# Performance work log

Measured on AMD Instinct MI355X. Metric: run time of the kernel, lower is better.

## Reference

```python
import jax, jax.numpy as jnp
import numpy as np

NEG_INF = -9e15  # matches the source's -9000000000000000.0 mask fill
ALPHA = 0.2      # leaky_relu negative slope


def setup_inputs() -> dict:
    key = jax.random.key(0)
    k1, k2, k3, k4 = jax.random.split(key, 4)
    B, N, C_IN, C_OUT, H = 2, 2048, 128, 128, 16
    c = C_OUT // H  # 8 per-head features; equals H//2 so source's a-slice is consistent
    node_feats = jax.random.normal(k1, (B, N, C_IN), dtype=jnp.float32)
    # random 0/1 adjacency with self-loops
    adj = jax.random.randint(k2, (B, N, N), 0, 2).astype(jnp.float32)
    adj = jnp.maximum(adj, jnp.eye(N, dtype=jnp.float32)[None])
    # glorot-uniform-ish params
    W = jax.random.normal(k3, (C_IN, H * c), dtype=jnp.float32) * np.sqrt(2.0 / (C_IN + H * c))
    b = jnp.zeros((H * c,), dtype=jnp.float32)
    a = jax.random.normal(k4, (H, 2 * c), dtype=jnp.float32) * np.sqrt(2.0 / (H + 2 * c))
    return {"node_feats": node_feats, "adj_matrix": adj, "W": W, "b": b, "a": a}


def reference(node_feats, adj_matrix, W, b, a):
    B, N = node_feats.shape[:2]
    H = a.shape[0]
    c = a.shape[1] // 2
    # projection + split into heads: [B, N, H, c]
    h = (node_feats @ W + b).reshape(B, N, H, c)
    # additive attention halves (source slices a along last axis)
    logit_parent = jnp.einsum('bnhc,hc->bnh', h, a[:, :c])
    logit_child = jnp.einsum('bnhc,hc->bnh', h, a[:, c:])
    # dense broadcast-add logits: [B, N(i), N(j), H]
    attn_logits = logit_parent[:, :, None, :] + logit_child[:, None, :, :]
    attn_logits = jax.nn.leaky_relu(attn_logits, negative_slope=ALPHA)
    attn_logits = jnp.where(adj_matrix[..., None] == 1.0, attn_logits, NEG_INF)
    attn_probs = jax.nn.softmax(attn_logits, axis=2)  # over source nodes j
    out = jnp.einsum('bijh,bjhc->bihc', attn_probs, h)
    out = out.reshape(B, N, H * c)  # concat_heads=True
    return out, adj_matrix
```

## Files before the change

### kernel.cpp

```cpp
#include <hip/hip_runtime.h>
#include <hip/hip_bf16.h>


#define B_   2
#define N_   2048
#define CIN_ 128
#define H_   16

typedef _Float16 h2  __attribute__((ext_vector_type(2)));
typedef _Float16 v8h __attribute__((ext_vector_type(8)));
typedef float    v4f __attribute__((ext_vector_type(4)));

#define SC6 0.015625f

__device__ inline h2 pk_f16(float a, float b) {
  return __builtin_bit_cast(h2, __builtin_amdgcn_cvt_pkrtz(a, b));
}
__device__ inline unsigned as_u32(h2 v) { return __builtin_bit_cast(unsigned, v); }
__device__ inline h2 as_h2(unsigned u) { return __builtin_bit_cast(h2, u); }

__device__ inline unsigned mask4(float4 f) {
  unsigned r = (unsigned)f.x | ((unsigned)f.y << 8) |
               ((unsigned)f.z << 16) | ((unsigned)f.w << 24);
  return (r << 8) - r;
}

__global__ __launch_bounds__(128) void proj_kernel(
    const float* __restrict__ nf, const float* __restrict__ W,
    const float* __restrict__ bias, const float* __restrict__ a,
    unsigned* __restrict__ hQ, unsigned* __restrict__ qI,
    float* __restrict__ lpT, unsigned* __restrict__ ones) {
  const int row0 = blockIdx.x * 4;
  const int t    = threadIdx.x;
  if (blockIdx.x == 0) {
    ones[t] = 0x3C003C00u; ones[t + 128] = 0x3C003C00u;
    ones[t + 256] = 0x3C003C00u; ones[t + 384] = 0x3C003C00u;
  }
  __shared__ float sNf[4][CIN_];
  ((float4*)&sNf[0][0])[t] = ((const float4*)(nf + (long)row0 * CIN_))[t];
  __syncthreads();
  float acc[4];
  const float bv = bias[t];
#pragma unroll
  for (int r = 0; r < 4; ++r) acc[r] = bv;
#pragma unroll 8
  for (int k = 0; k < CIN_; ++k) {
    const float w = W[k * 128 + t];
#pragma unroll
    for (int r = 0; r < 4; ++r) acc[r] = fmaf(sNf[r][k], w, acc[r]);
  }
  const int h = t >> 3, kc = t & 7;
  const int b = row0 >> 11, n0 = row0 & (N_ - 1);
  const int bh = b * H_ + h;
  const int cdw = n0 >> 1;
  uint2 hv;
  hv.x = as_u32(pk_f16(acc[0], acc[1]));
  hv.y = as_u32(pk_f16(acc[2], acc[3]));
  *(uint2*)(hQ + ((long)(bh * 8 + kc)) * (N_ / 2) + cdw) = hv;

  const float ap = a[h * 16 + kc], ac = a[h * 16 + 8 + kc];
  float lpv[4], lcv[4];
#pragma unroll
  for (int r = 0; r < 4; ++r) {
    float x = acc[r] * ap, y = acc[r] * ac;
#pragma unroll
    for (int s = 1; s < 8; s <<= 1) {
      x += __shfl_xor(x, s);
      y += __shfl_xor(y, s);
    }
    lpv[r] = x; lcv[r] = y;
  }
  if (kc == 0) {
    float4 l0 = {lpv[0], lpv[1], lpv[2], lpv[3]};
    *(float4*)(lpT + (long)bh * N_ + n0) = l0;
    uint2 q1, q2;
    q1.x = as_u32(pk_f16(__expf(lcv[0]) * SC6, __expf(lcv[1]) * SC6));
    q1.y = as_u32(pk_f16(__expf(lcv[2]) * SC6, __expf(lcv[3]) * SC6));
    q2.x = as_u32(pk_f16(__expf(0.2f * lcv[0]) * SC6, __expf(0.2f * lcv[1]) * SC6));
    q2.y = as_u32(pk_f16(__expf(0.2f * lcv[2]) * SC6, __expf(0.2f * lcv[3]) * SC6));
    const int addr = bh * 2048 + (cdw >> 4) * 32 + ((cdw >> 2) & 3) * 8;
    const int off  = cdw & 3;
    *(uint2*)(qI + addr + off)     = q1;
    *(uint2*)(qI + addr + 4 + off) = q2;
  }
}

__global__ __launch_bounds__(512, 6) void attn_kernel(
    const float* __restrict__ adj, const unsigned* __restrict__ hQ,
    const unsigned* __restrict__ qI, const float* __restrict__ lpT,
    const unsigned* __restrict__ ones, float* __restrict__ pA,
    float* __restrict__ pL, float* __restrict__ adj_out) {
  const int jq   = blockIdx.x & 3;
  const int rest = blockIdx.x >> 2;
  const int b    = rest >> 7;
  const int i0   = (rest & 127) * 16;
  const int tid  = threadIdx.x;
  const int w    = tid >> 6;
  const int lane = tid & 63;

  __shared__ uint2    sAm[1024];
  __shared__ unsigned sQ[8192];

  {
    const int head = tid >> 5;
    const int off  = (tid & 31) * 16;
    const uint4* src = (const uint4*)(qI + (b * H_ + head) * 2048 + jq * 512 + off);
    uint4* dst = (uint4*)(sQ + head * 512 + off);
    dst[0] = src[0]; dst[1] = src[1]; dst[2] = src[2]; dst[3] = src[3];
  }
  {
    const long aoff = (long)(b * N_ + i0) * N_ + jq * 512;
    const float* abase = adj + aoff;
    float* obase = adj_out + aoff;
    float4 fa[2], fb[2];
    int rowv[2], ccv[2];
#pragma unroll
    for (int s = 0; s < 2; ++s) {
      const int D = s * 512 + tid;
      const int mm = D & 15, qc = D >> 4;
      ccv[s] = (qc >> 2) * 32 + (qc & 3) * 8;
      rowv[s] = mm;
      fa[s] = *(const float4*)(abase + (long)mm * N_ + ccv[s]);
      fb[s] = *(const float4*)(abase + (long)mm * N_ + ccv[s] + 4);
    }
#pragma unroll
    for (int s = 0; s < 2; ++s) {
      const int D = s * 512 + tid;
      uint2 mv; mv.x = mask4(fa[s]); mv.y = mask4(fb[s]);
      sAm[D] = mv;
      *(float4*)(obase + (long)rowv[s] * N_ + ccv[s])     = fa[s];
      *(float4*)(obase + (long)rowv[s] * N_ + ccv[s] + 4) = fb[s];
    }
  }
  __syncthreads();

  const int m  = lane & 15;
  const int q  = lane >> 4;
  const int bh0 = b * H_ + w;
  const int bh1 = bh0 + 8;

  const float lp0 = lpT[(long)bh0 * N_ + i0 + m];
  const float lp1 = lpT[(long)bh1 * N_ + i0 + m];
  const float e10 = __expf(lp0) * SC6, e20 = __expf(0.2f * lp0) * SC6;
  const float e11 = __expf(lp1) * SC6, e21 = __expf(0.2f * lp1) * SC6;
  const h2 P10 = pk_f16(e10, e10), P20 = pk_f16(e20, e20);
  const h2 P11 = pk_f16(e11, e11), P21 = pk_f16(e21, e21);

  const unsigned* sq0 = sQ + w * 512 + q * 8;
  const unsigned* sq1 = sQ + (w + 8) * 512 + q * 8;
  const unsigned* hp0 = (m < 8)
      ? hQ + ((long)(bh0 * 8 + m)) * (N_ / 2) + jq * 256 + q * 4
      : ones + q * 4;
  const unsigned* hp1 = (m < 8)
      ? hQ + ((long)(bh1 * 8 + m)) * (N_ / 2) + jq * 256 + q * 4
      : ones + q * 4;

  v4f acc0 = {0.f, 0.f, 0.f, 0.f};
  v4f acc1 = {0.f, 0.f, 0.f, 0.f};

  uint4 h0[2], h1[2];
  h0[0] = *(const uint4*)(hp0);      h1[0] = *(const uint4*)(hp1);
  h0[1] = *(const uint4*)(hp0 + 16); h1[1] = *(const uint4*)(hp1 + 16);

  for (int t2 = 0; t2 < 8; ++t2) {
#pragma unroll
    for (int s = 0; s < 2; ++s) {
      const int ch = t2 * 2 + s;
      const int pf = ((ch + 2) & 15) * 16;
      const uint4 n0 = *(const uint4*)(hp0 + pf);
      const uint4 n1 = *(const uint4*)(hp1 + pf);

      const uint4 q1c0 = *(const uint4*)(sq0 + ch * 32);
      const uint4 q2c0 = *(const uint4*)(sq0 + ch * 32 + 4);
      const uint4 q1c1 = *(const uint4*)(sq1 + ch * 32);
      const uint4 q2c1 = *(const uint4*)(sq1 + ch * 32 + 4);

      const uint2 Mv = sAm[ch * 64 + lane];
      const unsigned ma = __builtin_amdgcn_perm(Mv.x, Mv.x, 0x01010000u);
      const unsigned mb = __builtin_amdgcn_perm(Mv.x, Mv.x, 0x03030202u);
      const unsigned mc = __builtin_amdgcn_perm(Mv.y, Mv.y, 0x01010000u);
      const unsigned md = __builtin_amdgcn_perm(Mv.y, Mv.y, 0x03030202u);

      {
        const v8h bf = __builtin_bit_cast(v8h, h0[s]);
        const uint4 af = {
          as_u32(__builtin_elementwise_max(P10 * as_h2(q1c0.x), P20 * as_h2(q2c0.x))) & ma,
          as_u32(__builtin_elementwise_max(P10 * as_h2(q1c0.y), P20 * as_h2(q2c0.y))) & mb,
          as_u32(__builtin_elementwise_max(P10 * as_h2(q1c0.z), P20 * as_h2(q2c0.z))) & mc,
          as_u32(__builtin_elementwise_max(P10 * as_h2(q1c0.w), P20 * as_h2(q2c0.w))) & md};
        acc0 = __builtin_amdgcn_mfma_f32_16x16x32_f16(
            __builtin_bit_cast(v8h, af), bf, acc0, 0, 0, 0);
      }
      {
        const v8h bf = __builtin_bit_cast(v8h, h1[s]);
        const uint4 af = {
          as_u32(__builtin_elementwise_max(P11 * as_h2(q1c1.x), P21 * as_h2(q2c1.x))) & ma,
          as_u32(__builtin_elementwise_max(P11 * as_h2(q1c1.y), P21 * as_h2(q2c1.y))) & mb,
          as_u32(__builtin_elementwise_max(P11 * as_h2(q1c1.z), P21 * as_h2(q2c1.z))) & mc,
          as_u32(__builtin_elementwise_max(P11 * as_h2(q1c1.w), P21 * as_h2(q2c1.w))) & md};
        acc1 = __builtin_amdgcn_mfma_f32_16x16x32_f16(
            __builtin_bit_cast(v8h, af), bf, acc1, 0, 0, 0);
      }
      h0[s] = n0; h1[s] = n1;
    }
  }

#pragma unroll
  for (int g = 0; g < 2; ++g) {
    const int hw = g * 8 + w;
    const v4f av = g ? acc1 : acc0;
#pragma unroll
    for (int r = 0; r < 4; ++r) {
      const int gidx = (b * N_ + i0 + q * 4 + r) * H_ + hw;
      if (m < 8)  pA[jq * 524288 + (long)gidx * 8 + m] = av[r];
      if (m == 8) pL[jq * 65536 + gidx] = av[r];
    }
  }
}

__global__ __launch_bounds__(512) void combine_kernel(
    const float* __restrict__ pA, const float* __restrict__ pL,
    float* __restrict__ out) {
  const int g = blockIdx.x * 512 + threadIdx.x;
  const int gl = g >> 3;
  const float s = pL[gl] + pL[gl + 65536] + pL[gl + 131072] + pL[gl + 196608];
  const float v = pA[g] + pA[g + 524288] + pA[g + 1048576] + pA[g + 1572864];
  out[g] = v / s;
}

extern "C" void kernel_launch(void* const* d_in, const int* in_sizes, int n_in,
                              void* d_out, int out_size, void* d_ws, size_t ws_size,
                              hipStream_t stream) {
  const float* nf   = (const float*)d_in[0];
  const float* adj  = (const float*)d_in[1];
  const float* W    = (const float*)d_in[2];
  const float* bias = (const float*)d_in[3];
  const float* a    = (const float*)d_in[4];

  float* out     = (float*)d_out;
  float* adj_out = out + (long)B_ * N_ * H_ * 8;

  unsigned* ws   = (unsigned*)d_ws;
  unsigned* hQ   = ws;
  unsigned* qI   = ws + 262144;
  float*    lpT  = (float*)(ws + 327680);
  unsigned* ones = ws + 393216;
  float*    pA   = (float*)(ws + 393728);
  float*    pL   = (float*)(ws + 2490880);

  hipLaunchKernelGGL(proj_kernel, dim3(B_ * N_ / 4), dim3(128), 0, stream,
                     nf, W, bias, a, hQ, qI, lpT, ones);
  hipLaunchKernelGGL(attn_kernel, dim3(B_ * (N_ / 16) * 4), dim3(512), 0,
                     stream, adj, hQ, qI, lpT, ones, pA, pL, adj_out);
  hipLaunchKernelGGL(combine_kernel, dim3(1024), dim3(512), 0, stream,
                     pA, pL, out);
}
```

Baseline: 127.0 us.

## Process full key range per block, drop split-K combine kernel

The attention kernel now gives each block 32 query rows and 4 heads over the full source range, instead of a quarter of the keys for 16 rows and all 16 heads. Adjacency tiles are staged through shared memory in four stages, with the next stage's global loads overlapped with the MFMA work on the current one. Normalisation happens in-register through a lane shuffle, which removes the partial-sum buffers and the separate combine kernel. In exchange, each block re-reads its 32-row adjacency slab for every head group (four times in total), and the grid drops to 512 blocks of 256 threads, which lowers parallelism.

```diff
diff --git a/kernel.cpp b/kernel.cpp
--- a/kernel.cpp
+++ b/kernel.cpp
@@ -85,147 +85,144 @@
   }
 }
 
-__global__ __launch_bounds__(512, 6) void attn_kernel(
+__global__ __launch_bounds__(256) void attn_kernel(
     const float* __restrict__ adj, const unsigned* __restrict__ hQ,
     const unsigned* __restrict__ qI, const float* __restrict__ lpT,
-    const unsigned* __restrict__ ones, float* __restrict__ pA,
-    float* __restrict__ pL, float* __restrict__ adj_out) {
-  const int jq   = blockIdx.x & 3;
-  const int rest = blockIdx.x >> 2;
-  const int b    = rest >> 7;
-  const int i0   = (rest & 127) * 16;
-  const int tid  = threadIdx.x;
-  const int w    = tid >> 6;
-  const int lane = tid & 63;
-
-  __shared__ uint2    sAm[1024];
-  __shared__ unsigned sQ[8192];
-
-  {
-    const int head = tid >> 5;
-    const int off  = (tid & 31) * 16;
-    const uint4* src = (const uint4*)(qI + (b * H_ + head) * 2048 + jq * 512 + off);
-    uint4* dst = (uint4*)(sQ + head * 512 + off);
-    dst[0] = src[0]; dst[1] = src[1]; dst[2] = src[2]; dst[3] = src[3];
-  }
-  {
-    const long aoff = (long)(b * N_ + i0) * N_ + jq * 512;
-    const float* abase = adj + aoff;
-    float* obase = adj_out + aoff;
-    float4 fa[2], fb[2];
-    int rowv[2], ccv[2];
-#pragma unroll
-    for (int s = 0; s < 2; ++s) {
-      const int D = s * 512 + tid;
-      const int mm = D & 15, qc = D >> 4;
-      ccv[s] = (qc >> 2) * 32 + (qc & 3) * 8;
-      rowv[s] = mm;
-      fa[s] = *(const float4*)(abase + (long)mm * N_ + ccv[s]);
-      fb[s] = *(const float4*)(abase + (long)mm * N_ + ccv[s] + 4);
-    }
-#pragma unroll
-    for (int s = 0; s < 2; ++s) {
-      const int D = s * 512 + tid;
-      uint2 mv; mv.x = mask4(fa[s]); mv.y = mask4(fb[s]);
-      sAm[D] = mv;
-      *(float4*)(obase + (long)rowv[s] * N_ + ccv[s])     = fa[s];
-      *(float4*)(obase + (long)rowv[s] * N_ + ccv[s] + 4) = fb[s];
-    }
-  }
-  __syncthreads();
-
-  const int m  = lane & 15;
-  const int q  = lane >> 4;
-  const int bh0 = b * H_ + w;
-  const int bh1 = bh0 + 8;
-
-  const float lp0 = lpT[(long)bh0 * N_ + i0 + m];
-  const float lp1 = lpT[(long)bh1 * N_ + i0 + m];
-  const float e10 = __expf(lp0) * SC6, e20 = __expf(0.2f * lp0) * SC6;
-  const float e11 = __expf(lp1) * SC6, e21 = __expf(0.2f * lp1) * SC6;
-  const h2 P10 = pk_f16(e10, e10), P20 = pk_f16(e20, e20);
-  const h2 P11 = pk_f16(e11, e11), P21 = pk_f16(e21, e21);
-
-  const unsigned* sq0 = sQ + w * 512 + q * 8;
-  const unsigned* sq1 = sQ + (w + 8) * 512 + q * 8;
-  const unsigned* hp0 = (m < 8)
-      ? hQ + ((long)(bh0 * 8 + m)) * (N_ / 2) + jq * 256 + q * 4
+    const unsigned* __restrict__ ones, float* __restrict__ out,
+    float* __restrict__ adj_out) {
+  const int hg   = blockIdx.x & 3;
+  const int it   = (blockIdx.x >> 2) & 63;
+  const int b    = blockIdx.x >> 8;
+  const int i0   = it * 32;
+  const int t    = threadIdx.x;
+  const int w    = t >> 6;
+  const int lane = t & 63;
+  const int m    = lane & 15;
+  const int q    = lane >> 4;
+  const int h    = hg * 4 + w;
+  const int bh   = b * H_ + h;
+
+  __shared__ uint2 sAm[8192];
+
+  const int  tm = t & 15, tq = t >> 4;
+  const long abase = ((long)(b * N_) + i0) * N_;
+
+  float4 fa[2][4], fb[2][4];
+  auto STAGE_LOAD = [&](int ss) {
+#pragma unroll
+    for (int u = 0; u < 2; ++u)
+#pragma unroll
+      for (int k = 0; k < 4; ++k) {
+        const int qc  = ss * 64 + k * 16 + tq;
+        const int col = qc * 8;
+        const float* ap = adj + abase + (long)(u * 16 + tm) * N_ + col;
+        fa[u][k] = *(const float4*)(ap);
+        fb[u][k] = *(const float4*)(ap + 4);
+      }
+  };
+  auto STAGE_WRITE = [&](int ss) {
+    const bool docopy = (ss == hg);
+#pragma unroll
+    for (int u = 0; u < 2; ++u)
+#pragma unroll
+      for (int k = 0; k < 4; ++k) {
+        uint2 mv;
+        mv.x = mask4(fa[u][k]); mv.y = mask4(fb[u][k]);
+        sAm[u * 4096 + ss * 1024 + k * 256 + t] = mv;
+        if (docopy) {
+          const int qc  = ss * 64 + k * 16 + tq;
+          const int col = qc * 8;
+          float* op = adj_out + abase + (long)(u * 16 + tm) * N_ + col;
+          *(float4*)(op)     = fa[u][k];
+          *(float4*)(op + 4) = fb[u][k];
+        }
+      }
+  };
+
+  const float lpa = lpT[(long)bh * N_ + i0 + m];
+  const float lpb = lpT[(long)bh * N_ + i0 + 16 + m];
+  const float e1a = __expf(lpa) * SC6, e2a = __expf(0.2f * lpa) * SC6;
+  const float e1b = __expf(lpb) * SC6, e2b = __expf(0.2f * lpb) * SC6;
+  const h2 P1a = pk_f16(e1a, e1a), P2a = pk_f16(e2a, e2a);
+  const h2 P1b = pk_f16(e1b, e1b), P2b = pk_f16(e2b, e2b);
+
+  const unsigned* qp = qI + bh * 2048 + q * 8;
+  const unsigned hmask = (m < 8) ? ~0u : 0u;
+  const unsigned* hp = (m < 8)
+      ? hQ + ((long)(bh * 8 + m)) * (N_ / 2) + q * 4
       : ones + q * 4;
-  const unsigned* hp1 = (m < 8)
-      ? hQ + ((long)(bh1 * 8 + m)) * (N_ / 2) + jq * 256 + q * 4
-      : ones + q * 4;
+
+  uint4 bq1[2], bq2[2], bhq[2];
+  bq1[0] = *(const uint4*)(qp);       bq2[0] = *(const uint4*)(qp + 4);
+  bq1[1] = *(const uint4*)(qp + 32);  bq2[1] = *(const uint4*)(qp + 36);
+  bhq[0] = *(const uint4*)(hp);
+  bhq[1] = *(const uint4*)(hp + (16 & hmask));
 
   v4f acc0 = {0.f, 0.f, 0.f, 0.f};
   v4f acc1 = {0.f, 0.f, 0.f, 0.f};
 
-  uint4 h0[2], h1[2];
-  h0[0] = *(const uint4*)(hp0);      h1[0] = *(const uint4*)(hp1);
-  h0[1] = *(const uint4*)(hp0 + 16); h1[1] = *(const uint4*)(hp1 + 16);
-
-  for (int t2 = 0; t2 < 8; ++t2) {
-#pragma unroll
-    for (int s = 0; s < 2; ++s) {
-      const int ch = t2 * 2 + s;
-      const int pf = ((ch + 2) & 15) * 16;
-      const uint4 n0 = *(const uint4*)(hp0 + pf);
-      const uint4 n1 = *(const uint4*)(hp1 + pf);
-
-      const uint4 q1c0 = *(const uint4*)(sq0 + ch * 32);
-      const uint4 q2c0 = *(const uint4*)(sq0 + ch * 32 + 4);
-      const uint4 q1c1 = *(const uint4*)(sq1 + ch * 32);
-      const uint4 q2c1 = *(const uint4*)(sq1 + ch * 32 + 4);
-
-      const uint2 Mv = sAm[ch * 64 + lane];
-      const unsigned ma = __builtin_amdgcn_perm(Mv.x, Mv.x, 0x01010000u);
-      const unsigned mb = __builtin_amdgcn_perm(Mv.x, Mv.x, 0x03030202u);
-      const unsigned mc = __builtin_amdgcn_perm(Mv.y, Mv.y, 0x01010000u);
-      const unsigned md = __builtin_amdgcn_perm(Mv.y, Mv.y, 0x03030202u);
-
-      {
-        const v8h bf = __builtin_bit_cast(v8h, h0[s]);
-        const uint4 af = {
-          as_u32(__builtin_elementwise_max(P10 * as_h2(q1c0.x), P20 * as_h2(q2c0.x))) & ma,
-          as_u32(__builtin_elementwise_max(P10 * as_h2(q1c0.y), P20 * as_h2(q2c0.y))) & mb,
-          as_u32(__builtin_elementwise_max(P10 * as_h2(q1c0.z), P20 * as_h2(q2c0.z))) & mc,
-          as_u32(__builtin_elementwise_max(P10 * as_h2(q1c0.w), P20 * as_h2(q2c0.w))) & md};
-        acc0 = __builtin_amdgcn_mfma_f32_16x16x32_f16(
-            __builtin_bit_cast(v8h, af), bf, acc0, 0, 0, 0);
+  STAGE_LOAD(0);
+  STAGE_WRITE(0);
+  __syncthreads();
+
+  for (int s = 0; s < 4; ++s) {
+    if (s < 3) STAGE_LOAD(s + 1);
+#pragma unroll
+    for (int cc = 0; cc < 16; ++cc) {
+      const int ch = s * 16 + cc;
+      const int p  = ch & 1;
+      const uint4 nq1 = *(const uint4*)(qp + (ch + 2) * 32);
+      const uint4 nq2 = *(const uint4*)(qp + (ch + 2) * 32 + 4);
+      const uint4 nhq = *(const uint4*)(hp + (((ch + 2) * 16) & hmask));
+
+      const uint2 Mv0 = sAm[ch * 64 + lane];
+      const uint2 Mv1 = sAm[4096 + ch * 64 + lane];
+      const unsigned m0a = __builtin_amdgcn_perm(Mv0.x, Mv0.x, 0x01010000u);
+      const unsigned m0b = __builtin_amdgcn_perm(Mv0.x, Mv0.x, 0x03030202u);
+      const unsigned m0c = __builtin_amdgcn_perm(Mv0.y, Mv0.y, 0x01010000u);
+      const unsigned m0d = __builtin_amdgcn_perm(Mv0.y, Mv0.y, 0x03030202u);
+      const unsigned m1a = __builtin_amdgcn_perm(Mv1.x, Mv1.x, 0x01010000u);
+      const unsigned m1b = __builtin_amdgcn_perm(Mv1.x, Mv1.x, 0x03030202u);
+      const unsigned m1c = __builtin_amdgcn_perm(Mv1.y, Mv1.y, 0x01010000u);
+      const unsigned m1d = __builtin_amdgcn_perm(Mv1.y, Mv1.y, 0x03030202u);
+
+      const uint4 q1 = bq1[p], q2 = bq2[p];
+      const h2 Q1x = as_h2(q1.x), Q1y = as_h2(q1.y), Q1z = as_h2(q1.z), Q1w = as_h2(q1.w);
+      const h2 Q2x = as_h2(q2.x), Q2y = as_h2(q2.y), Q2z = as_h2(q2.z), Q2w = as_h2(q2.w);
+      const v8h bf = __builtin_bit_cast(v8h, bhq[p]);
+
+      const uint4 af0 = {
+        as_u32(__builtin_elementwise_max(P1a * Q1x, P2a * Q2x)) & m0a,
+        as_u32(__builtin_elementwise_max(P1a * Q1y, P2a * Q2y)) & m0b,
+        as_u32(__builtin_elementwise_max(P1a * Q1z, P2a * Q2z)) & m0c,
+        as_u32(__builtin_elementwise_max(P1a * Q1w, P2a * Q2w)) & m0d};
+      acc0 = __builtin_amdgcn_mfma_f32_16x16x32_f16(
+          __builtin_bit_cast(v8h, af0), bf, acc0, 0, 0, 0);
+      const uint4 af1 = {
+        as_u32(__builtin_elementwise_max(P1b * Q1x, P2b * Q2x)) & m1a,
+        as_u32(__builtin_elementwise_max(P1b * Q1y, P2b * Q2y)) & m1b,
+        as_u32(__builtin_elementwise_max(P1b * Q1z, P2b * Q2z)) & m1c,
+        as_u32(__builtin_elementwise_max(P1b * Q1w, P2b * Q2w)) & m1d};
+      acc1 = __builtin_amdgcn_mfma_f32_16x16x32_f16(
+          __builtin_bit_cast(v8h, af1), bf, acc1, 0, 0, 0);
+
+      bq1[p] = nq1; bq2[p] = nq2; bhq[p] = nhq;
+    }
+    if (s < 3) { STAGE_WRITE(s + 1); __syncthreads(); }
+  }
+
+#pragma unroll
+  for (int u = 0; u < 2; ++u) {
+    const v4f av = u ? acc1 : acc0;
+#pragma unroll
+    for (int r = 0; r < 4; ++r) {
+      const float sden = __shfl(av[r], (lane & 48) | 8);
+      if (m < 8) {
+        const long gi = ((long)(b * N_ + i0 + u * 16 + q * 4 + r)) * H_ + h;
+        out[gi * 8 + m] = av[r] / sden;
       }
-      {
-        const v8h bf = __builtin_bit_cast(v8h, h1[s]);
-        const uint4 af = {
-          as_u32(__builtin_elementwise_max(P11 * as_h2(q1c1.x), P21 * as_h2(q2c1.x))) & ma,
-          as_u32(__builtin_elementwise_max(P11 * as_h2(q1c1.y), P21 * as_h2(q2c1.y))) & mb,
-          as_u32(__builtin_elementwise_max(P11 * as_h2(q1c1.z), P21 * as_h2(q2c1.z))) & mc,
-          as_u32(__builtin_elementwise_max(P11 * as_h2(q1c1.w), P21 * as_h2(q2c1.w))) & md};
-        acc1 = __builtin_amdgcn_mfma_f32_16x16x32_f16(
-            __builtin_bit_cast(v8h, af), bf, acc1, 0, 0, 0);
-      }
-      h0[s] = n0; h1[s] = n1;
     }
   }
-
-#pragma unroll
-  for (int g = 0; g < 2; ++g) {
-    const int hw = g * 8 + w;
-    const v4f av = g ? acc1 : acc0;
-#pragma unroll
-    for (int r = 0; r < 4; ++r) {
-      const int gidx = (b * N_ + i0 + q * 4 + r) * H_ + hw;
-      if (m < 8)  pA[jq * 524288 + (long)gidx * 8 + m] = av[r];
-      if (m == 8) pL[jq * 65536 + gidx] = av[r];
-    }
-  }
-}
-
-__global__ __launch_bounds__(512) void combine_kernel(
-    const float* __restrict__ pA, const float* __restrict__ pL,
-    float* __restrict__ out) {
-  const int g = blockIdx.x * 512 + threadIdx.x;
-  const int gl = g >> 3;
-  const float s = pL[gl] + pL[gl + 65536] + pL[gl + 131072] + pL[gl + 196608];
-  const float v = pA[g] + pA[g + 524288] + pA[g + 1048576] + pA[g + 1572864];
-  out[g] = v / s;
 }
 
 extern "C" void kernel_launch(void* const* d_in, const int* in_sizes, int n_in,
@@ -245,13 +242,9 @@
   unsigned* qI   = ws + 262144;
   float*    lpT  = (float*)(ws + 327680);
   unsigned* ones = ws + 393216;
-  float*    pA   = (float*)(ws + 393728);
-  float*    pL   = (float*)(ws + 2490880);
 
   hipLaunchKernelGGL(proj_kernel, dim3(B_ * N_ / 4), dim3(128), 0, stream,
                      nf, W, bias, a, hQ, qI, lpT, ones);
-  hipLaunchKernelGGL(attn_kernel, dim3(B_ * (N_ / 16) * 4), dim3(512), 0,
-                     stream, adj, hQ, qI, lpT, ones, pA, pL, adj_out);
-  hipLaunchKernelGGL(combine_kernel, dim3(1024), dim3(512), 0, stream,
-                     pA, pL, out);
-}
+  hipLaunchKernelGGL(attn_kernel, dim3(B_ * 64 * 4), dim3(256), 0,
+                     stream, adj, hQ, qI, lpT, ones, out, adj_out);
+}
```

Measured after the change: 139.5 us. 1.1x slower.
